# Kernel tuning notes

Hardware: AMD Instinct MI355X
Metric: run time of the kernel (lower is better)

## Reference

```python
import jax, jax.numpy as jnp
import numpy as np

NUM_GROUPS = 128
GROUP_SIZE = 1024
N_POINTS = 262144


def setup_inputs() -> dict:
    key = jax.random.key(0)
    k1, k2, k3, k4 = jax.random.split(key, 4)
    point_cloud = jax.random.normal(k1, (1, 3, N_POINTS), dtype=jnp.float32)
    # pointwise-MLP feature extractor params (3 -> 64 -> 128 -> 1024)
    w1 = jax.random.normal(k2, (3, 64), dtype=jnp.float32) * 0.1
    w2 = jax.random.normal(k3, (64, 128), dtype=jnp.float32) * 0.1
    w3 = jax.random.normal(k4, (128, 1024), dtype=jnp.float32) * 0.03
    return {"point_cloud": point_cloud, "w1": w1, "w2": w2, "w3": w3}


def _fps(points, num_groups):
    # points: [N, 3]. Seed = point farthest from the centroid (as in source),
    # then iterative farthest-point sampling. The source recomputes distances
    # to every sampled point each step; keeping a running min-distance is
    # mathematically identical.
    centroid = points.mean(axis=0, keepdims=True)
    d0 = jnp.linalg.norm(points - centroid, axis=1)  # [N]
    first = jnp.argmax(d0)
    min_dist = jnp.linalg.norm(points - points[first], axis=1)  # [N]

    def step(min_dist, _):
        nxt = jnp.argmax(min_dist)
        d = jnp.linalg.norm(points - points[nxt], axis=1)
        return jnp.minimum(min_dist, d), nxt

    _, idx_rest = jax.lax.scan(step, min_dist, None, length=num_groups - 1)
    return jnp.concatenate([first[None], idx_rest])  # [G]


def reference(point_cloud, w1, w2, w3):
    pc = point_cloud[0].T  # [N, 3]  (squeeze(0).permute(1,0))
    fps_idx = _fps(pc, NUM_GROUPS)
    sampled = pc[fps_idx]  # [G, 3]
    # Brute-force KNN (sklearn kneighbors equivalent): squared dists [G, N]
    d2 = (jnp.sum(sampled * sampled, axis=1, keepdims=True)
          - 2.0 * (sampled @ pc.T)
          + jnp.sum(pc * pc, axis=1)[None, :])
    _, knn_idx = jax.lax.top_k(-d2, GROUP_SIZE)  # [G, K] nearest indices
    groups = pc[knn_idx]  # [G, K, 3] irregular gather
    # feature_: per-point MLP + max-pool over the K points of each patch.
    # (Pointwise op => batching all G groups at once equals the source's
    # pairwise batched calls.)
    h = jax.nn.relu(groups @ w1)       # [G, K, 64]
    h = jax.nn.relu(h @ w2)            # [G, K, 128]
    h = h @ w3                         # [G, K, 1024]
    patch_features = h.max(axis=1)     # [G, 1024]
    return patch_features, sampled
```

## Files before the change

kernel.cpp:

```cpp
#include <hip/hip_runtime.h>

#define N_PTS 262144
#define NG 128
#define GS 1024
#define FPS_B 16

typedef __attribute__((ext_vector_type(8))) short short8;
typedef __attribute__((ext_vector_type(8))) __bf16 bf16x8;
typedef __attribute__((ext_vector_type(4))) float f32x4;
typedef unsigned long long ull;

__device__ __forceinline__ unsigned short f2bf(float f) {
  unsigned u = __float_as_uint(f);
  unsigned r = u + 0x7FFFu + ((u >> 16) & 1u);
  return (unsigned short)(r >> 16);
}

__device__ __forceinline__ f32x4 mfma16(short8 a, short8 b, f32x4 c) {
  return __builtin_amdgcn_mfma_f32_16x16x32_bf16(
      __builtin_bit_cast(bf16x8, a), __builtin_bit_cast(bf16x8, b), c, 0, 0, 0);
}

__device__ __forceinline__ ull shfl_xor_u64(ull v, int m) {
  unsigned lo = __shfl_xor((unsigned)v, m);
  unsigned hi = __shfl_xor((unsigned)(v >> 32), m);
  return ((ull)hi << 32) | lo;
}

__device__ __forceinline__ void st64(ull* p, ull v) {
  __hip_atomic_store(p, v, __ATOMIC_RELAXED, __HIP_MEMORY_SCOPE_AGENT);
}
__device__ __forceinline__ ull ld64(const ull* p) {
  return __hip_atomic_load(p, __ATOMIC_RELAXED, __HIP_MEMORY_SCOPE_AGENT);
}

__device__ __forceinline__ unsigned ordenc(float f) {
  unsigned u = __float_as_uint(f);
  return (u >> 31) ? ~u : (u | 0x80000000u);
}

__device__ __forceinline__ unsigned knn_key(float x, float y, float z, float pp,
                                            float sx, float sy, float sz, float s2) {
  float dot = __fmaf_rn(sx, x, __fmaf_rn(sy, y, __fmul_rn(sz, z)));
  float d2 = __fadd_rn(__fsub_rn(s2, __fadd_rn(dot, dot)), pp);
  return ordenc(d2);
}

__global__ void __launch_bounds__(1024) fps_kernel(const float* __restrict__ pc,
    const float* __restrict__ w2, const float* __restrict__ w3,
    unsigned short* __restrict__ w2t, unsigned short* __restrict__ w3t,
    float* __restrict__ sampled_out, unsigned* __restrict__ cnts,
    ull* __restrict__ kslots, ull* __restrict__ cslots) {
  const int tid = threadIdx.x;
  if (blockIdx.x >= FPS_B) {
    const int pb = blockIdx.x - FPS_B;
    int i3 = pb * 1024 + tid;
    { int n = i3 >> 7, k = i3 & 127; w3t[i3] = f2bf(w3[k * 1024 + n]); }
    if (pb < 8) { int i2 = pb * 1024 + tid; int n = i2 >> 6, k = i2 & 63; w2t[i2] = f2bf(w2[k * 128 + n]); }
    return;
  }
  const int p = blockIdx.x;
  const int lane = tid & 63, wv = tid >> 6;
  const int gt = p * 1024 + tid;
  const float* xs = pc;
  const float* ys = pc + N_PTS;
  const float* zs = pc + 2 * N_PTS;
  float x[16], y[16], z[16], md[16];
  float sx = 0.f, sy = 0.f, sz = 0.f;
#pragma unroll
  for (int j = 0; j < 16; ++j) {
    int i = gt + j * 16384;
    x[j] = xs[i]; y[j] = ys[i]; z[j] = zs[i];
    sx += x[j]; sy += y[j]; sz += z[j];
  }
#pragma unroll
  for (int m = 32; m; m >>= 1) {
    sx += __shfl_xor(sx, m); sy += __shfl_xor(sy, m); sz += __shfl_xor(sz, m);
  }
  __shared__ float rs[3][16];
  __shared__ ull wkeyL[16];
  __shared__ float bc[3];
  if (lane == 0) { rs[0][wv] = sx; rs[1][wv] = sy; rs[2][wv] = sz; }
  __syncthreads();
  if (tid == 0) {
    float ax = 0.f, ay = 0.f, az = 0.f;
    for (int w = 0; w < 16; ++w) { ax += rs[0][w]; ay += rs[1][w]; az += rs[2][w]; }
    st64(&cslots[0 + p], (ull)__float_as_uint(ax));
    st64(&cslots[16 + p], (ull)__float_as_uint(ay));
    st64(&cslots[32 + p], (ull)__float_as_uint(az));
    __hip_atomic_fetch_add(&cnts[4], 1u, __ATOMIC_RELEASE, __HIP_MEMORY_SCOPE_AGENT);
  }
  if (wv == 0) {
    while (__hip_atomic_load(&cnts[4], __ATOMIC_RELAXED, __HIP_MEMORY_SCOPE_AGENT) < 16u)
      __builtin_amdgcn_s_sleep(1);
    (void)__hip_atomic_load(&cnts[4], __ATOMIC_ACQUIRE, __HIP_MEMORY_SCOPE_AGENT);
    float f = 0.f;
    if (lane < 48) f = __uint_as_float((unsigned)ld64(&cslots[lane]));
    float s = 0.f;
    for (int q = 0; q < 16; ++q) s += __shfl(f, (lane & 48) + q);
    if (lane == 0)  bc[0] = s * (1.f / N_PTS);
    if (lane == 16) bc[1] = s * (1.f / N_PTS);
    if (lane == 32) bc[2] = s * (1.f / N_PTS);
  }
  __syncthreads();
  ull lkey = 0ull;
  {
    float cx = bc[0], cy = bc[1], cz = bc[2];
#pragma unroll
    for (int j = 0; j < 16; ++j) {
      float dx = x[j] - cx, dy = y[j] - cy, dz = z[j] - cz;
      float d = __fmaf_rn(dx, dx, __fmaf_rn(dy, dy, dz * dz));
      md[j] = d;
      unsigned fb = __float_as_uint(d);
      ull k = ((ull)fb << 18) | (ull)(0x3FFFFu ^ (unsigned)(gt + j * 16384));
      if (k > lkey) lkey = k;
    }
  }
  for (int sel = 0; sel < NG; ++sel) {
    const ull seq = (ull)(sel + 1);
    ull rk = lkey;
#pragma unroll
    for (int m = 32; m; m >>= 1) {
      ull o = shfl_xor_u64(rk, m);
      if (o > rk) rk = o;
    }
    if (lane == 0) wkeyL[wv] = rk;
    __syncthreads();
    if (wv == 0) {
      const int pb = (sel & 1) * 16;
      ull bk = (lane < 16) ? wkeyL[lane] : 0ull;
#pragma unroll
      for (int m = 8; m; m >>= 1) {
        ull o = shfl_xor_u64(bk, m);
        if (o > bk) bk = o;
      }
      if (lane == 0) st64(&kslots[pb + p], (seq << 50) | bk);
      ull v = 0ull; float c = 0.f;
      bool got = (lane >= 48);
      for (;;) {
        if (!got) {
          v = ld64(&kslots[pb + (lane & 15)]);
          if ((v >> 50) == seq) {
            got = true;
            unsigned idx = 0x3FFFFu ^ (unsigned)(v & 0x3FFFFull);
            c = pc[(lane >> 4) * N_PTS + idx];
          }
        }
        if (__all((int)got)) break;
      }
      ull gk = v;
      int ws_ = lane & 15;
#pragma unroll
      for (int m = 8; m; m >>= 1) {
        ull o = shfl_xor_u64(gk, m);
        int ow = __shfl_xor(ws_, m);
        if (o > gk) { gk = o; ws_ = ow; }
      }
      if (lane < 48 && (lane & 15) == ws_) {
        bc[lane >> 4] = c;
        if (p == 0) sampled_out[sel * 3 + (lane >> 4)] = c;
      }
    }
    __syncthreads();
    {
      float wx = bc[0], wy = bc[1], wz = bc[2];
      ull nk = 0ull;
#pragma unroll
      for (int j = 0; j < 16; ++j) {
        float dx = x[j] - wx, dy = y[j] - wy, dz = z[j] - wz;
        float d = __fmaf_rn(dx, dx, __fmaf_rn(dy, dy, dz * dz));
        float m = (sel == 0) ? d : fminf(md[j], d);
        md[j] = m;
        unsigned fb = __float_as_uint(m);
        ull k = ((ull)fb << 18) | (ull)(0x3FFFFu ^ (unsigned)(gt + j * 16384));
        if (k > nk) nk = k;
      }
      lkey = nk;
    }
  }
}

__device__ __forceinline__ void select_bucket(const unsigned* hist, int nbins,
                                              unsigned krem, unsigned* sres, int lane) {
  const int per = nbins >> 6;
  unsigned local = 0;
  for (int j = 0; j < per; ++j) local += hist[lane * per + j];
  unsigned inc = local;
  for (int off = 1; off < 64; off <<= 1) {
    unsigned v = __shfl_up(inc, off);
    if (lane >= off) inc += v;
  }
  unsigned exc = inc - local;
  if (exc < krem && krem <= inc) {
    unsigned c = exc;
    for (int j = 0; j < per; ++j) {
      unsigned h = hist[lane * per + j];
      if (c + h >= krem) { sres[0] = (unsigned)(lane * per + j); sres[1] = c; break; }
      c += h;
    }
  }
}

__global__ void __launch_bounds__(1024) knn_kernel(const float* __restrict__ pc,
    const float* __restrict__ sampled, int* __restrict__ knn) {
  const int g = blockIdx.x;
  const int tid = threadIdx.x;
  const int lane = tid & 63;
  __shared__ unsigned hist[2048];
  __shared__ unsigned candk[8192];
  __shared__ unsigned candi[8192];
  __shared__ unsigned candk2[2048];
  __shared__ unsigned candi2[2048];
  __shared__ unsigned sres[2];
  __shared__ unsigned scnt[6];
  const f32x4* xs4 = (const f32x4*)pc;
  const f32x4* ys4 = (const f32x4*)(pc + N_PTS);
  const f32x4* zs4 = (const f32x4*)(pc + 2 * N_PTS);
  const float sx = sampled[g * 3 + 0], sy = sampled[g * 3 + 1], sz = sampled[g * 3 + 2];
  const float s2 = __fadd_rn(__fadd_rn(__fmul_rn(sx, sx), __fmul_rn(sy, sy)),
                             __fmul_rn(sz, sz));
  for (int i = tid; i < 2048; i += 1024) hist[i] = 0u;
  if (tid < 6) scnt[tid] = 0u;
  __syncthreads();
  for (int it = 0; it < 4; ++it) {
    int i4 = it * 1024 + tid;
    f32x4 xv = xs4[i4], yv = ys4[i4], zv = zs4[i4];
#pragma unroll
    for (int u = 0; u < 4; ++u) {
      float pp = __fadd_rn(__fadd_rn(__fmul_rn(xv[u], xv[u]), __fmul_rn(yv[u], yv[u])),
                           __fmul_rn(zv[u], zv[u]));
      unsigned k = knn_key(xv[u], yv[u], zv[u], pp, sx, sy, sz, s2);
      atomicAdd(&hist[k >> 21], 1u);
    }
  }
  __syncthreads();
  if (tid < 64) select_bucket(hist, 2048, 160u, sres, lane);
  __syncthreads();
  const unsigned Tp = (sres[0] >= 2047u) ? 0xFFFFFFFFu : ((sres[0] + 1u) << 21);
  __syncthreads();
  for (int it = 0; it < 64; ++it) {
    int i4 = it * 1024 + tid;
    f32x4 xv = xs4[i4], yv = ys4[i4], zv = zs4[i4];
#pragma unroll
    for (int u = 0; u < 4; ++u) {
      float pp = __fadd_rn(__fadd_rn(__fmul_rn(xv[u], xv[u]), __fmul_rn(yv[u], yv[u])),
                           __fmul_rn(zv[u], zv[u]));
      unsigned k = knn_key(xv[u], yv[u], zv[u], pp, sx, sy, sz, s2);
      if (k < Tp) {
        unsigned e = atomicAdd(&scnt[0], 1u);
        if (e < 8192u) { candk[e] = k; candi[e] = (unsigned)(i4 * 4 + u); }
      }
    }
  }
  __syncthreads();
  const int m = (int)min(scnt[0], 8192u);
  for (int i = tid; i < 2048; i += 1024) hist[i] = 0u;
  __syncthreads();
  for (int j = tid; j < m; j += 1024) atomicAdd(&hist[candk[j] >> 21], 1u);
  __syncthreads();
  if (tid < 64) select_bucket(hist, 2048, GS, sres, lane);
  __syncthreads();
  const unsigned bA = sres[0];
  unsigned krem = GS - sres[1];
  __syncthreads();
  for (int j = tid; j < m; j += 1024) {
    unsigned k = candk[j], b = k >> 21;
    if (b < bA) {
      unsigned pos = atomicAdd(&scnt[1], 1u);
      knn[g * GS + (int)pos] = (int)candi[j];
    } else if (b == bA) {
      unsigned e = atomicAdd(&scnt[2], 1u);
      if (e < 2048u) { candk2[e] = k; candi2[e] = candi[j]; }
    }
  }
  __syncthreads();
  const int m2 = (int)min(scnt[2], 2048u);
  const int base1 = (int)scnt[1];
  for (int i = tid; i < 2048; i += 1024) hist[i] = 0u;
  __syncthreads();
  for (int j = tid; j < m2; j += 1024) atomicAdd(&hist[(candk2[j] >> 10) & 2047u], 1u);
  __syncthreads();
  if (tid < 64) select_bucket(hist, 2048, krem, sres, lane);
  __syncthreads();
  const unsigned bB = sres[0];
  krem -= sres[1];
  __syncthreads();
  if (tid < 1024) hist[tid] = 0u;
  __syncthreads();
  for (int j = tid; j < m2; j += 1024)
    if (((candk2[j] >> 10) & 2047u) == bB) atomicAdd(&hist[candk2[j] & 1023u], 1u);
  __syncthreads();
  if (tid < 64) select_bucket(hist, 1024, krem, sres, lane);
  __syncthreads();
  const unsigned bC = sres[0];
  krem -= sres[1];
  const unsigned T = (bA << 21) | (bB << 10) | bC;
  __syncthreads();
  for (int j = tid; j < m2; j += 1024) {
    unsigned k = candk2[j];
    if (k < T) {
      unsigned pos = atomicAdd(&scnt[3], 1u);
      knn[g * GS + base1 + (int)pos] = (int)candi2[j];
    } else if (k == T) {
      unsigned e = atomicAdd(&scnt[4], 1u);
      if (e < 2048u) hist[e] = candi2[j];
    }
  }
  __syncthreads();
  if (tid < 64) {
    const int tc = (int)min(scnt[4], 2048u);
    const int base2 = base1 + (int)scnt[3];
    for (int j = 0; j < (int)krem; ++j) {
      int best = 0x7FFFFFFF;
      for (int q = lane; q < tc; q += 64) best = min(best, (int)hist[q]);
      for (int mm = 32; mm; mm >>= 1) best = min(best, __shfl_xor(best, mm));
      for (int q = lane; q < tc; q += 64)
        if ((int)hist[q] == best) hist[q] = 0x7FFFFFFFu;
      if (lane == 0) knn[g * GS + base2 + j] = best;
    }
  }
}

__global__ void __launch_bounds__(256, 2) mlp_kernel(const float* __restrict__ pc,
    const int* __restrict__ knn, const float* __restrict__ w1,
    const unsigned short* __restrict__ w2t, const unsigned short* __restrict__ w3t,
    unsigned* __restrict__ gout) {
  const int blk = blockIdx.x, g = blk >> 2, split = blk & 3;
  const int tid = threadIdx.x, lane = tid & 63, wv = tid >> 6;
  __shared__ unsigned gmax[1024];
  __shared__ __align__(16) short h1[128 * 72];
  __shared__ __align__(16) short h2[128 * 136];
  __shared__ float cxs[128], cys[128], czs[128];
  for (int i = tid; i < 1024; i += 256) gmax[i] = 0u;
  const float* xs = pc;
  const float* ys = pc + N_PTS;
  const float* zs = pc + 2 * N_PTS;
  const int ch = tid & 63;
  const int pgrp = tid >> 6;
  const float w10 = w1[ch], w11 = w1[64 + ch], w12 = w1[128 + ch];
  const int r0 = (lane >> 4) * 4;
  const int cB = lane & 15;
  const int kB = (lane >> 4) * 8;
  for (int tile = 0; tile < 2; ++tile) {
    __syncthreads();
    if (tid < 128) {
      int i = knn[g * 1024 + split * 256 + tile * 128 + tid];
      cxs[tid] = xs[i]; cys[tid] = ys[i]; czs[tid] = zs[i];
    }
    __syncthreads();
    for (int q = 0; q < 32; ++q) {
      int p = pgrp * 32 + q;
      float v = fmaxf(__fmaf_rn(cxs[p], w10, __fmaf_rn(cys[p], w11, czs[p] * w12)), 0.f);
      h1[p * 72 + ch] = (short)f2bf(v);
    }
    __syncthreads();
    {
      short8 a[2][2];
#pragma unroll
      for (int mt = 0; mt < 2; ++mt)
#pragma unroll
        for (int ks = 0; ks < 2; ++ks)
          a[mt][ks] = *(const short8*)&h1[((2 * wv + mt) * 16 + cB) * 72 + kB + ks * 32];
#pragma unroll
      for (int n0 = 0; n0 < 8; ++n0) {
        short8 bb[2];
#pragma unroll
        for (int ks = 0; ks < 2; ++ks)
          bb[ks] = *(const short8*)&w2t[(n0 * 16 + cB) * 64 + kB + ks * 32];
#pragma unroll
        for (int mt = 0; mt < 2; ++mt) {
          f32x4 acc = {0.f, 0.f, 0.f, 0.f};
          acc = mfma16(a[mt][0], bb[0], acc);
          acc = mfma16(a[mt][1], bb[1], acc);
          int rr = (2 * wv + mt) * 16 + r0;
#pragma unroll
          for (int r = 0; r < 4; ++r)
            h2[(rr + r) * 136 + n0 * 16 + cB] = (short)f2bf(fmaxf(acc[r], 0.f));
        }
      }
    }
    __syncthreads();
    {
      short8 a2[2][4];
#pragma unroll
      for (int mt = 0; mt < 2; ++mt)
#pragma unroll
        for (int ks = 0; ks < 4; ++ks)
          a2[mt][ks] = *(const short8*)&h2[((2 * wv + mt) * 16 + cB) * 136 + kB + ks * 32];
      for (int n0 = 0; n0 < 64; ++n0) {
        short8 b3[4];
#pragma unroll
        for (int ks = 0; ks < 4; ++ks)
          b3[ks] = *(const short8*)&w3t[(n0 * 16 + cB) * 128 + kB + ks * 32];
        f32x4 acc0 = {0.f, 0.f, 0.f, 0.f}, acc1 = {0.f, 0.f, 0.f, 0.f};
#pragma unroll
        for (int ks = 0; ks < 4; ++ks) acc0 = mfma16(a2[0][ks], b3[ks], acc0);
#pragma unroll
        for (int ks = 0; ks < 4; ++ks) acc1 = mfma16(a2[1][ks], b3[ks], acc1);
        float mv = fmaxf(fmaxf(fmaxf(acc0[0], acc0[1]), fmaxf(acc0[2], acc0[3])),
                         fmaxf(fmaxf(acc1[0], acc1[1]), fmaxf(acc1[2], acc1[3])));
        mv = fmaxf(mv, __shfl_xor(mv, 16));
        mv = fmaxf(mv, __shfl_xor(mv, 32));
        if (lane < 16) atomicMax(&gmax[n0 * 16 + lane], ordenc(mv));
      }
    }
  }
  __syncthreads();
  for (int i = tid; i < 1024; i += 256)
    gout[(g * 4 + split) * 1024 + i] = gmax[i];
}

__global__ void __launch_bounds__(256) combine_kernel(const unsigned* __restrict__ gm,
                                                      float* __restrict__ out) {
  int c = blockIdx.x * 256 + threadIdx.x;
  int g = c >> 10, chn = c & 1023;
  unsigned m = 0u;
#pragma unroll
  for (int s = 0; s < 4; ++s) {
    unsigned v = gm[(g * 4 + s) * 1024 + chn];
    if (v > m) m = v;
  }
  out[c] = (m >> 31) ? __uint_as_float(m ^ 0x80000000u) : __uint_as_float(~m);
}

extern "C" void kernel_launch(void* const* d_in, const int* in_sizes, int n_in,
                              void* d_out, int out_size, void* d_ws, size_t ws_size,
                              hipStream_t stream) {
  (void)in_sizes; (void)n_in; (void)out_size; (void)ws_size;
  const float* pc = (const float*)d_in[0];
  const float* w1 = (const float*)d_in[1];
  const float* w2 = (const float*)d_in[2];
  const float* w3 = (const float*)d_in[3];
  float* out = (float*)d_out;
  char* ws = (char*)d_ws;

  unsigned* cnts = (unsigned*)(ws + 0);
  ull* kslots = (ull*)(ws + 128);
  ull* cslots = (ull*)(ws + 1024);
  unsigned short* w2t = (unsigned short*)(ws + 4096);
  unsigned short* w3t = (unsigned short*)(ws + 4096 + 16384);
  int* knn = (int*)(ws + 4096 + 16384 + 262144);
  unsigned* gout = (unsigned*)(ws + 4096 + 16384 + 262144 + 524288);
  float* sampled = out + 131072;

  hipMemsetAsync(ws, 0, 4096, stream);
  fps_kernel<<<FPS_B + 128, 1024, 0, stream>>>(pc, w2, w3, w2t, w3t, sampled,
                                               cnts, kslots, cslots);
  knn_kernel<<<NG, 1024, 0, stream>>>(pc, sampled, knn);
  mlp_kernel<<<NG * 4, 256, 0, stream>>>(pc, knn, w1, w2t, w3t, gout);
  combine_kernel<<<512, 256, 0, stream>>>(gout, out);
}
```

Before: 585.0 us.

## Fuse KNN into FPS kernel with per-sample mailbox handoff

Merges the KNN kernel into the persistent FPS launch. The 128 extra blocks, which previously only transposed weights, now each spin on a global mailbox slot until FPS block 0 publishes that group's sampled point, then run the KNN selection. This lets KNN for early samples overlap the serial FPS iterations and removes one kernel launch boundary. The cost is that those blocks busy-wait while holding large shared memory, and forward progress depends on all FPS blocks and waiting blocks being co-resident.

```diff
diff --git a/kernel.cpp b/kernel.cpp
--- a/kernel.cpp
+++ b/kernel.cpp
@@ -46,21 +46,174 @@
   return ordenc(d2);
 }
 
-__global__ void __launch_bounds__(1024) fps_kernel(const float* __restrict__ pc,
+__device__ __forceinline__ void select_bucket(const unsigned* hist, int nbins,
+                                              unsigned krem, unsigned* sres, int lane) {
+  const int per = nbins >> 6;
+  unsigned local = 0;
+  for (int j = 0; j < per; ++j) local += hist[lane * per + j];
+  unsigned inc = local;
+  for (int off = 1; off < 64; off <<= 1) {
+    unsigned v = __shfl_up(inc, off);
+    if (lane >= off) inc += v;
+  }
+  unsigned exc = inc - local;
+  if (exc < krem && krem <= inc) {
+    unsigned c = exc;
+    for (int j = 0; j < per; ++j) {
+      unsigned h = hist[lane * per + j];
+      if (c + h >= krem) { sres[0] = (unsigned)(lane * per + j); sres[1] = c; break; }
+      c += h;
+    }
+  }
+}
+
+__global__ void __launch_bounds__(1024) fps_knn_kernel(const float* __restrict__ pc,
     const float* __restrict__ w2, const float* __restrict__ w3,
     unsigned short* __restrict__ w2t, unsigned short* __restrict__ w3t,
-    float* __restrict__ sampled_out, unsigned* __restrict__ cnts,
-    ull* __restrict__ kslots, ull* __restrict__ cslots) {
+    float* __restrict__ sampled_out, int* __restrict__ knn,
+    unsigned* __restrict__ cnts, ull* __restrict__ kslots, ull* __restrict__ mb,
+    ull* __restrict__ cslots) {
+  __shared__ __align__(16) char sbuf[90112];
+  __shared__ unsigned sres[2];
+  __shared__ unsigned scnt[6];
+  __shared__ float mbx[3];
+  __shared__ float rs[3][16];
+  __shared__ ull wkeyL[16];
+  __shared__ float bc[3];
   const int tid = threadIdx.x;
+  const int lane = tid & 63, wv = tid >> 6;
+
   if (blockIdx.x >= FPS_B) {
-    const int pb = blockIdx.x - FPS_B;
-    int i3 = pb * 1024 + tid;
-    { int n = i3 >> 7, k = i3 & 127; w3t[i3] = f2bf(w3[k * 1024 + n]); }
-    if (pb < 8) { int i2 = pb * 1024 + tid; int n = i2 >> 6, k = i2 & 63; w2t[i2] = f2bf(w2[k * 128 + n]); }
+    const int g = blockIdx.x - FPS_B;
+    {
+      int i3 = g * 1024 + tid;
+      { int n = i3 >> 7, k = i3 & 127; w3t[i3] = f2bf(w3[k * 1024 + n]); }
+      if (g < 8) { int i2 = g * 1024 + tid; int n = i2 >> 6, k = i2 & 63; w2t[i2] = f2bf(w2[k * 128 + n]); }
+    }
+    unsigned* hist = (unsigned*)sbuf;
+    unsigned* candk = (unsigned*)(sbuf + 8192);
+    unsigned* candi = (unsigned*)(sbuf + 40960);
+    unsigned* candk2 = (unsigned*)(sbuf + 73728);
+    unsigned* candi2 = (unsigned*)(sbuf + 81920);
+    for (int i = tid; i < 2048; i += 1024) hist[i] = 0u;
+    if (tid < 6) scnt[tid] = 0u;
+    if (tid < 3) {
+      ull v;
+      for (;;) {
+        v = ld64(&mb[g * 16 + tid]);
+        if ((unsigned)v == (unsigned)(g + 1)) break;
+        __builtin_amdgcn_s_sleep(64);
+      }
+      mbx[tid] = __uint_as_float((unsigned)(v >> 32));
+    }
+    __syncthreads();
+    const float sx = mbx[0], sy = mbx[1], sz = mbx[2];
+    const float s2 = __fadd_rn(__fadd_rn(__fmul_rn(sx, sx), __fmul_rn(sy, sy)),
+                               __fmul_rn(sz, sz));
+    const f32x4* xs4 = (const f32x4*)pc;
+    const f32x4* ys4 = (const f32x4*)(pc + N_PTS);
+    const f32x4* zs4 = (const f32x4*)(pc + 2 * N_PTS);
+    for (int it = 0; it < 4; ++it) {
+      int i4 = it * 1024 + tid;
+      f32x4 xv = xs4[i4], yv = ys4[i4], zv = zs4[i4];
+#pragma unroll
+      for (int u = 0; u < 4; ++u) {
+        float pp = __fadd_rn(__fadd_rn(__fmul_rn(xv[u], xv[u]), __fmul_rn(yv[u], yv[u])),
+                             __fmul_rn(zv[u], zv[u]));
+        unsigned k = knn_key(xv[u], yv[u], zv[u], pp, sx, sy, sz, s2);
+        atomicAdd(&hist[k >> 21], 1u);
+      }
+    }
+    __syncthreads();
+    if (tid < 64) select_bucket(hist, 2048, 160u, sres, lane);
+    __syncthreads();
+    const unsigned Tp = (sres[0] >= 2047u) ? 0xFFFFFFFFu : ((sres[0] + 1u) << 21);
+    __syncthreads();
+    for (int it = 0; it < 64; ++it) {
+      int i4 = it * 1024 + tid;
+      f32x4 xv = xs4[i4], yv = ys4[i4], zv = zs4[i4];
+#pragma unroll
+      for (int u = 0; u < 4; ++u) {
+        float pp = __fadd_rn(__fadd_rn(__fmul_rn(xv[u], xv[u]), __fmul_rn(yv[u], yv[u])),
+                             __fmul_rn(zv[u], zv[u]));
+        unsigned k = knn_key(xv[u], yv[u], zv[u], pp, sx, sy, sz, s2);
+        if (k < Tp) {
+          unsigned e = atomicAdd(&scnt[0], 1u);
+          if (e < 8192u) { candk[e] = k; candi[e] = (unsigned)(i4 * 4 + u); }
+        }
+      }
+    }
+    __syncthreads();
+    const int m = (int)min(scnt[0], 8192u);
+    for (int i = tid; i < 2048; i += 1024) hist[i] = 0u;
+    __syncthreads();
+    for (int j = tid; j < m; j += 1024) atomicAdd(&hist[candk[j] >> 21], 1u);
+    __syncthreads();
+    if (tid < 64) select_bucket(hist, 2048, GS, sres, lane);
+    __syncthreads();
+    const unsigned bA = sres[0];
+    unsigned krem = GS - sres[1];
+    __syncthreads();
+    for (int j = tid; j < m; j += 1024) {
+      unsigned k = candk[j], b = k >> 21;
+      if (b < bA) {
+        unsigned pos = atomicAdd(&scnt[1], 1u);
+        knn[g * GS + (int)pos] = (int)candi[j];
+      } else if (b == bA) {
+        unsigned e = atomicAdd(&scnt[2], 1u);
+        if (e < 2048u) { candk2[e] = k; candi2[e] = candi[j]; }
+      }
+    }
+    __syncthreads();
+    const int m2 = (int)min(scnt[2], 2048u);
+    const int base1 = (int)scnt[1];
+    for (int i = tid; i < 2048; i += 1024) hist[i] = 0u;
+    __syncthreads();
+    for (int j = tid; j < m2; j += 1024) atomicAdd(&hist[(candk2[j] >> 10) & 2047u], 1u);
+    __syncthreads();
+    if (tid < 64) select_bucket(hist, 2048, krem, sres, lane);
+    __syncthreads();
+    const unsigned bB = sres[0];
+    krem -= sres[1];
+    __syncthreads();
+    if (tid < 1024) hist[tid] = 0u;
+    __syncthreads();
+    for (int j = tid; j < m2; j += 1024)
+      if (((candk2[j] >> 10) & 2047u) == bB) atomicAdd(&hist[candk2[j] & 1023u], 1u);
+    __syncthreads();
+    if (tid < 64) select_bucket(hist, 1024, krem, sres, lane);
+    __syncthreads();
+    const unsigned bC = sres[0];
+    krem -= sres[1];
+    const unsigned T = (bA << 21) | (bB << 10) | bC;
+    __syncthreads();
+    for (int j = tid; j < m2; j += 1024) {
+      unsigned k = candk2[j];
+      if (k < T) {
+        unsigned pos = atomicAdd(&scnt[3], 1u);
+        knn[g * GS + base1 + (int)pos] = (int)candi2[j];
+      } else if (k == T) {
+        unsigned e = atomicAdd(&scnt[4], 1u);
+        if (e < 2048u) hist[e] = candi2[j];
+      }
+    }
+    __syncthreads();
+    if (tid < 64) {
+      const int tc = (int)min(scnt[4], 2048u);
+      const int base2 = base1 + (int)scnt[3];
+      for (int j = 0; j < (int)krem; ++j) {
+        int best = 0x7FFFFFFF;
+        for (int q = lane; q < tc; q += 64) best = min(best, (int)hist[q]);
+        for (int mm = 32; mm; mm >>= 1) best = min(best, __shfl_xor(best, mm));
+        for (int q = lane; q < tc; q += 64)
+          if ((int)hist[q] == best) hist[q] = 0x7FFFFFFFu;
+        if (lane == 0) knn[g * GS + base2 + j] = best;
+      }
+    }
     return;
   }
+
   const int p = blockIdx.x;
-  const int lane = tid & 63, wv = tid >> 6;
   const int gt = p * 1024 + tid;
   const float* xs = pc;
   const float* ys = pc + N_PTS;
@@ -77,9 +230,6 @@
   for (int m = 32; m; m >>= 1) {
     sx += __shfl_xor(sx, m); sy += __shfl_xor(sy, m); sz += __shfl_xor(sz, m);
   }
-  __shared__ float rs[3][16];
-  __shared__ ull wkeyL[16];
-  __shared__ float bc[3];
   if (lane == 0) { rs[0][wv] = sx; rs[1][wv] = sy; rs[2][wv] = sz; }
   __syncthreads();
   if (tid == 0) {
@@ -158,7 +308,10 @@
       }
       if (lane < 48 && (lane & 15) == ws_) {
         bc[lane >> 4] = c;
-        if (p == 0) sampled_out[sel * 3 + (lane >> 4)] = c;
+        if (p == 0) {
+          sampled_out[sel * 3 + (lane >> 4)] = c;
+          st64(&mb[sel * 16 + (lane >> 4)], ((ull)__float_as_uint(c) << 32) | seq);
+        }
       }
     }
     __syncthreads();
@@ -176,147 +329,6 @@
         if (k > nk) nk = k;
       }
       lkey = nk;
-    }
-  }
-}
-
-__device__ __forceinline__ void select_bucket(const unsigned* hist, int nbins,
-                                              unsigned krem, unsigned* sres, int lane) {
-  const int per = nbins >> 6;
-  unsigned local = 0;
-  for (int j = 0; j < per; ++j) local += hist[lane * per + j];
-  unsigned inc = local;
-  for (int off = 1; off < 64; off <<= 1) {
-    unsigned v = __shfl_up(inc, off);
-    if (lane >= off) inc += v;
-  }
-  unsigned exc = inc - local;
-  if (exc < krem && krem <= inc) {
-    unsigned c = exc;
-    for (int j = 0; j < per; ++j) {
-      unsigned h = hist[lane * per + j];
-      if (c + h >= krem) { sres[0] = (unsigned)(lane * per + j); sres[1] = c; break; }
-      c += h;
-    }
-  }
-}
-
-__global__ void __launch_bounds__(1024) knn_kernel(const float* __restrict__ pc,
-    const float* __restrict__ sampled, int* __restrict__ knn) {
-  const int g = blockIdx.x;
-  const int tid = threadIdx.x;
-  const int lane = tid & 63;
-  __shared__ unsigned hist[2048];
-  __shared__ unsigned candk[8192];
-  __shared__ unsigned candi[8192];
-  __shared__ unsigned candk2[2048];
-  __shared__ unsigned candi2[2048];
-  __shared__ unsigned sres[2];
-  __shared__ unsigned scnt[6];
-  const f32x4* xs4 = (const f32x4*)pc;
-  const f32x4* ys4 = (const f32x4*)(pc + N_PTS);
-  const f32x4* zs4 = (const f32x4*)(pc + 2 * N_PTS);
-  const float sx = sampled[g * 3 + 0], sy = sampled[g * 3 + 1], sz = sampled[g * 3 + 2];
-  const float s2 = __fadd_rn(__fadd_rn(__fmul_rn(sx, sx), __fmul_rn(sy, sy)),
-                             __fmul_rn(sz, sz));
-  for (int i = tid; i < 2048; i += 1024) hist[i] = 0u;
-  if (tid < 6) scnt[tid] = 0u;
-  __syncthreads();
-  for (int it = 0; it < 4; ++it) {
-    int i4 = it * 1024 + tid;
-    f32x4 xv = xs4[i4], yv = ys4[i4], zv = zs4[i4];
-#pragma unroll
-    for (int u = 0; u < 4; ++u) {
-      float pp = __fadd_rn(__fadd_rn(__fmul_rn(xv[u], xv[u]), __fmul_rn(yv[u], yv[u])),
-                           __fmul_rn(zv[u], zv[u]));
-      unsigned k = knn_key(xv[u], yv[u], zv[u], pp, sx, sy, sz, s2);
-      atomicAdd(&hist[k >> 21], 1u);
-    }
-  }
-  __syncthreads();
-  if (tid < 64) select_bucket(hist, 2048, 160u, sres, lane);
-  __syncthreads();
-  const unsigned Tp = (sres[0] >= 2047u) ? 0xFFFFFFFFu : ((sres[0] + 1u) << 21);
-  __syncthreads();
-  for (int it = 0; it < 64; ++it) {
-    int i4 = it * 1024 + tid;
-    f32x4 xv = xs4[i4], yv = ys4[i4], zv = zs4[i4];
-#pragma unroll
-    for (int u = 0; u < 4; ++u) {
-      float pp = __fadd_rn(__fadd_rn(__fmul_rn(xv[u], xv[u]), __fmul_rn(yv[u], yv[u])),
-                           __fmul_rn(zv[u], zv[u]));
-      unsigned k = knn_key(xv[u], yv[u], zv[u], pp, sx, sy, sz, s2);
-      if (k < Tp) {
-        unsigned e = atomicAdd(&scnt[0], 1u);
-        if (e < 8192u) { candk[e] = k; candi[e] = (unsigned)(i4 * 4 + u); }
-      }
-    }
-  }
-  __syncthreads();
-  const int m = (int)min(scnt[0], 8192u);
-  for (int i = tid; i < 2048; i += 1024) hist[i] = 0u;
-  __syncthreads();
-  for (int j = tid; j < m; j += 1024) atomicAdd(&hist[candk[j] >> 21], 1u);
-  __syncthreads();
-  if (tid < 64) select_bucket(hist, 2048, GS, sres, lane);
-  __syncthreads();
-  const unsigned bA = sres[0];
-  unsigned krem = GS - sres[1];
-  __syncthreads();
-  for (int j = tid; j < m; j += 1024) {
-    unsigned k = candk[j], b = k >> 21;
-    if (b < bA) {
-      unsigned pos = atomicAdd(&scnt[1], 1u);
-      knn[g * GS + (int)pos] = (int)candi[j];
-    } else if (b == bA) {
-      unsigned e = atomicAdd(&scnt[2], 1u);
-      if (e < 2048u) { candk2[e] = k; candi2[e] = candi[j]; }
-    }
-  }
-  __syncthreads();
-  const int m2 = (int)min(scnt[2], 2048u);
-  const int base1 = (int)scnt[1];
-  for (int i = tid; i < 2048; i += 1024) hist[i] = 0u;
-  __syncthreads();
-  for (int j = tid; j < m2; j += 1024) atomicAdd(&hist[(candk2[j] >> 10) & 2047u], 1u);
-  __syncthreads();
-  if (tid < 64) select_bucket(hist, 2048, krem, sres, lane);
-  __syncthreads();
-  const unsigned bB = sres[0];
-  krem -= sres[1];
-  __syncthreads();
-  if (tid < 1024) hist[tid] = 0u;
-  __syncthreads();
-  for (int j = tid; j < m2; j += 1024)
-    if (((candk2[j] >> 10) & 2047u) == bB) atomicAdd(&hist[candk2[j] & 1023u], 1u);
-  __syncthreads();
-  if (tid < 64) select_bucket(hist, 1024, krem, sres, lane);
-  __syncthreads();
-  const unsigned bC = sres[0];
-  krem -= sres[1];
-  const unsigned T = (bA << 21) | (bB << 10) | bC;
-  __syncthreads();
-  for (int j = tid; j < m2; j += 1024) {
-    unsigned k = candk2[j];
-    if (k < T) {
-      unsigned pos = atomicAdd(&scnt[3], 1u);
-      knn[g * GS + base1 + (int)pos] = (int)candi2[j];
-    } else if (k == T) {
-      unsigned e = atomicAdd(&scnt[4], 1u);
-      if (e < 2048u) hist[e] = candi2[j];
-    }
-  }
-  __syncthreads();
-  if (tid < 64) {
-    const int tc = (int)min(scnt[4], 2048u);
-    const int base2 = base1 + (int)scnt[3];
-    for (int j = 0; j < (int)krem; ++j) {
-      int best = 0x7FFFFFFF;
-      for (int q = lane; q < tc; q += 64) best = min(best, (int)hist[q]);
-      for (int mm = 32; mm; mm >>= 1) best = min(best, __shfl_xor(best, mm));
-      for (int q = lane; q < tc; q += 64)
-        if ((int)hist[q] == best) hist[q] = 0x7FFFFFFFu;
-      if (lane == 0) knn[g * GS + base2 + j] = best;
     }
   }
 }
@@ -437,16 +449,16 @@
   unsigned* cnts = (unsigned*)(ws + 0);
   ull* kslots = (ull*)(ws + 128);
   ull* cslots = (ull*)(ws + 1024);
-  unsigned short* w2t = (unsigned short*)(ws + 4096);
-  unsigned short* w3t = (unsigned short*)(ws + 4096 + 16384);
-  int* knn = (int*)(ws + 4096 + 16384 + 262144);
-  unsigned* gout = (unsigned*)(ws + 4096 + 16384 + 262144 + 524288);
+  ull* mb = (ull*)(ws + 2048);
+  unsigned short* w2t = (unsigned short*)(ws + 24576);
+  unsigned short* w3t = (unsigned short*)(ws + 24576 + 16384);
+  int* knn = (int*)(ws + 24576 + 16384 + 262144);
+  unsigned* gout = (unsigned*)(ws + 24576 + 16384 + 262144 + 524288);
   float* sampled = out + 131072;
 
-  hipMemsetAsync(ws, 0, 4096, stream);
-  fps_kernel<<<FPS_B + 128, 1024, 0, stream>>>(pc, w2, w3, w2t, w3t, sampled,
-                                               cnts, kslots, cslots);
-  knn_kernel<<<NG, 1024, 0, stream>>>(pc, sampled, knn);
+  hipMemsetAsync(ws, 0, 20480, stream);
+  fps_knn_kernel<<<FPS_B + NG, 1024, 0, stream>>>(pc, w2, w3, w2t, w3t, sampled,
+                                                  knn, cnts, kslots, mb, cslots);
   mlp_kernel<<<NG * 4, 256, 0, stream>>>(pc, knn, w1, w2t, w3t, gout);
   combine_kernel<<<512, 256, 0, stream>>>(gout, out);
 }
```

Result: no change. 576.1 us, median of 2 (-1.5%).
